# Kernel optimization log

Hardware: AMD Instinct MI355X
Metric: run time of the kernel (lower is better)

## Reference

```python
import jax, jax.numpy as jnp
import numpy as np

DN = ('NCHW', 'OIHW', 'NCHW')
K = 7          # window_size
PAD = K // 2   # 3
GC = 32
CIN = 1
COUT = 3
DIM = 128
RED = DIM // 4  # reduction=4 -> 32


def conv3x3(x, w, b):
    out = jax.lax.conv_general_dilated(x, w, (1, 1), [(1, 1), (1, 1)],
                                       dimension_numbers=DN)
    return out + b[None, :, None, None]


def lrelu(x):
    return jnp.where(x >= 0, x, 0.2 * x)


def setup_inputs() -> dict:
    key = jax.random.key(0)
    ks = jax.random.split(key, 18)
    def n(k, shape, s=0.05):
        return jax.random.normal(k, shape, dtype=jnp.float32) * s
    return {
        'x': jax.random.normal(ks[0], (8, CIN, 256, 256), dtype=jnp.float32),
        'c1_w': n(ks[1], (GC, CIN, 3, 3)),            'c1_b': n(ks[2], (GC,)),
        'c2_w': n(ks[3], (GC, CIN + GC, 3, 3)),       'c2_b': n(ks[4], (GC,)),
        'c3_w': n(ks[5], (GC, CIN + 2 * GC, 3, 3)),   'c3_b': n(ks[6], (GC,)),
        'c4_w': n(ks[7], (GC - 1, CIN + 3 * GC, 3, 3)), 'c4_b': n(ks[8], (GC - 1,)),
        # DynamicDWConv squeeze-excite weight generator
        'dw_w1': n(ks[9], (RED, DIM)),                # 1x1 conv, no bias
        'dw_bn_g': jnp.ones((RED,), jnp.float32),      # BN gamma (eval mode)
        'dw_bn_b': jnp.zeros((RED,), jnp.float32),     # BN beta
        'dw_w2': n(ks[10], (DIM * K * K, RED)),        'dw_b2': n(ks[11], (DIM * K * K,)),
        'dw_bias': n(ks[12], (DIM,)),                  # per-channel bias of depthwise conv
        'c5_w': n(ks[13], (COUT, DIM, 3, 3)),          'c5_b': n(ks[14], (COUT,)),
    }


def reference(x, c1_w, c1_b, c2_w, c2_b, c3_w, c3_b, c4_w, c4_b,
              dw_w1, dw_bn_g, dw_bn_b, dw_w2, dw_b2, dw_bias, c5_w, c5_b):
    # residual dense block
    x1 = lrelu(conv3x3(x, c1_w, c1_b))
    x2 = lrelu(conv3x3(jnp.concatenate((x, x1), 1), c2_w, c2_b))
    x3 = lrelu(conv3x3(jnp.concatenate((x, x1, x2), 1), c3_w, c3_b))
    x4 = lrelu(conv3x3(jnp.concatenate((x, x1, x2, x3), 1), c4_w, c4_b))
    feat = jnp.concatenate((x, x1, x2, x3, x4), 1)  # [b, 128, h, w]
    b = feat.shape[0]

    # DynamicDWConv: generate per-sample depthwise kernels via squeeze-excite
    pooled = feat.mean(axis=(2, 3))                            # [b, 128]
    h = jax.nn.relu(pooled @ dw_w1.T * dw_bn_g + dw_bn_b)      # BN(eval: mean=0,var=1)
    wgen = h @ dw_w2.T + dw_b2                                 # [b, 128*K*K]
    wdw = wgen.reshape(b, DIM, 1, K, K)                        # per-sample dw kernels

    def dw_one(xi, wi):  # xi: [128,h,w], wi: [128,1,K,K]
        return jax.lax.conv_general_dilated(
            xi[None], wi, (1, 1), [(PAD, PAD), (PAD, PAD)],
            dimension_numbers=DN, feature_group_count=DIM)[0]

    dw_out = jax.vmap(dw_one)(feat, wdw) + dw_bias[None, :, None, None]
    x45 = lrelu(dw_out)
    return conv3x3(x45, c5_w, c5_b)
```

## Files before the change

### kernel.cpp

```cpp
#include <hip/hip_runtime.h>
#include <hip/hip_bf16.h>


typedef _Float16 f16;
typedef _Float16 f16x2 __attribute__((ext_vector_type(2)));
typedef _Float16 f16x8 __attribute__((ext_vector_type(8)));
typedef float f32x16 __attribute__((ext_vector_type(16)));

#define IMG 256
#define HW 65536
#define CH 128

static __device__ __forceinline__ size_t fidx(int b, int h, int w) {
    return (((size_t)b * IMG + h) * IMG + w) * CH;
}

__global__ __launch_bounds__(256) void prep_wt_k(const float* __restrict__ src,
                                                 f16* __restrict__ dst,
                                                 int Cin, int COUT) {
    int idx = blockIdx.x * 256 + threadIdx.x;
    if (idx >= 9 * 32 * 128) return;
    int tap = idx >> 12;
    int oc  = (idx >> 7) & 31;
    int pc  = idx & 127;
    int ic  = (pc == 127) ? 0 : pc + 1;
    float v = 0.f;
    if (oc < COUT && ic < Cin) v = src[(oc * Cin + ic) * 9 + tap];
    dst[idx] = (f16)v;
}

__global__ __launch_bounds__(256) void conv1_k(const float* __restrict__ x,
                                               f16* __restrict__ feat,
                                               const float* __restrict__ w,
                                               const float* __restrict__ bias) {
    int wx = threadIdx.x, h = blockIdx.x & 255, b = blockIdx.x >> 8;
    const float* p = x + (size_t)b * HW + h * IMG;
    bool hm = h > 0, hp = h < 255, wm = wx > 0, wp = wx < 255;
    float v[9];
    v[0] = (hm && wm) ? p[wx - 1 - IMG] : 0.f;
    v[1] = hm ? p[wx - IMG] : 0.f;
    v[2] = (hm && wp) ? p[wx + 1 - IMG] : 0.f;
    v[3] = wm ? p[wx - 1] : 0.f;
    v[4] = p[wx];
    v[5] = wp ? p[wx + 1] : 0.f;
    v[6] = (hp && wm) ? p[wx - 1 + IMG] : 0.f;
    v[7] = hp ? p[wx + IMG] : 0.f;
    v[8] = (hp && wp) ? p[wx + 1 + IMG] : 0.f;

    float acc[32];
#pragma unroll
    for (int oc = 0; oc < 32; ++oc) {
        float s = bias[oc];
#pragma unroll
        for (int k = 0; k < 9; ++k) s = fmaf(v[k], w[oc * 9 + k], s);
        acc[oc] = (s >= 0.f) ? s : 0.2f * s;
    }
    f16* op = feat + fidx(b, h, wx);
#pragma unroll
    for (int oc = 0; oc < 32; oc += 2) {
        f16x2 pr = {(f16)acc[oc], (f16)acc[oc + 1]};
        *(f16x2*)(op + oc) = pr;
    }
    op[127] = (f16)v[4];
}

#define NSTT 10
#define STT (18 * 34 * 32)

__device__ __forceinline__ void stage_issue_t(const f16* __restrict__ src,
                                              int b, int r0, int w0, int c0,
                                              int tid, f16x8* v) {
#pragma unroll
    for (int it = 0; it < NSTT; ++it) {
        int u = tid + it * 256;
        int r = u / 136, rem = u - r * 136;
        int slot = rem >> 2, cg = rem & 3;
        int gh = r0 - 1 + r, gw = w0 - 1 + slot;
        bool ok = (u < 2448) && ((unsigned)gh < 256u) && ((unsigned)gw < 256u);
        int ch = gh < 0 ? 0 : (gh > 255 ? 255 : gh);
        int cw = gw < 0 ? 0 : (gw > 255 ? 255 : gw);
        f16x8 t = *(const f16x8*)(src + fidx(b, ch, cw) + c0 + cg * 8);
        f16x8 z = {};
        v[it] = ok ? t : z;
    }
}

__device__ __forceinline__ void stage_write_t(f16* __restrict__ St, int tid,
                                              const f16x8* v) {
#pragma unroll
    for (int it = 0; it < NSTT; ++it) {
        int u = tid + it * 256;
        if (u < 2448) {
            int r = u / 136, rem = u - r * 136;
            int slot = rem >> 2, cg = rem & 3;
            *(f16x8*)(St + ((r * 34 + slot) * 4 + (cg ^ ((slot >> 1) & 3))) * 8) = v[it];
        }
    }
}

__device__ __forceinline__ void compute_t(const f16* __restrict__ St,
                                          const f16* __restrict__ Wt, int c0,
                                          int wave, int l31, int g,
                                          f32x16* acc) {
#pragma unroll
    for (int kx = 0; kx < 3; ++kx) {
        f16x8 A0[3], A1[3];
#pragma unroll
        for (int ky = 0; ky < 3; ++ky) {
            const f16* wp = Wt + ((ky * 3 + kx) * 32 + l31) * 128 + c0 + g * 8;
            A0[ky] = *(const f16x8*)(wp);
            A1[ky] = *(const f16x8*)(wp + 16);
        }
        int slot = l31 + kx;
        int sw = (slot >> 1) & 3;
        int base = wave * 4;
        f16x8 B0[3], B1[3];
#pragma unroll
        for (int i = 0; i < 2; ++i) {
            int rb = ((base + i) * 34 + slot) * 4;
            B0[i] = *(const f16x8*)(St + (rb + ((0 + g) ^ sw)) * 8);
            B1[i] = *(const f16x8*)(St + (rb + ((2 + g) ^ sw)) * 8);
        }
#pragma unroll
        for (int r = 0; r < 4; ++r) {
            int rb = ((base + r + 2) * 34 + slot) * 4;
            B0[(r + 2) % 3] = *(const f16x8*)(St + (rb + ((0 + g) ^ sw)) * 8);
            B1[(r + 2) % 3] = *(const f16x8*)(St + (rb + ((2 + g) ^ sw)) * 8);
#pragma unroll
            for (int ky = 0; ky < 3; ++ky) {
                acc[r] = __builtin_amdgcn_mfma_f32_32x32x16_f16(A0[ky], B0[(r + ky) % 3], acc[r], 0, 0, 0);
                acc[r] = __builtin_amdgcn_mfma_f32_32x32x16_f16(A1[ky], B1[(r + ky) % 3], acc[r], 0, 0, 0);
            }
        }
    }
}

__global__ __launch_bounds__(256, 2) void convm_k(f16* __restrict__ feat,
                                                  const f16* __restrict__ Wt,
                                                  const float* __restrict__ bias,
                                                  int outbase, int cmask, int COUT) {
    __shared__ f16 St[STT];
    int tid = threadIdx.x;
    int wave = tid >> 6, lane = tid & 63;
    int l31 = lane & 31, g = lane >> 5;
    int bi = blockIdx.x;
    int b = bi & 7;
    int tile = bi >> 3;
    int pxt = tile & 7, rt = tile >> 3;
    int r0 = rt * 16;
    int w0 = pxt * 32;
    f32x16 acc[4] = {{}, {}, {}, {}};

    for (int ck = 0; ck < 4; ++ck) {
        if (!((cmask >> ck) & 1)) continue;
        int c0 = ck * 32;
        f16x8 v[NSTT];
        stage_issue_t(feat, b, r0, w0, c0, tid, v);
        stage_write_t(St, tid, v);
        __syncthreads();
        compute_t(St, Wt, c0, wave, l31, g, acc);
        __syncthreads();
    }

    int px = w0 + l31;
#pragma unroll
    for (int r = 0; r < 4; ++r) {
        f16* op = feat + fidx(b, r0 + wave * 4 + r, px) + outbase;
#pragma unroll
        for (int q = 0; q < 16; q += 2) {
            int oc0 = (q & 3) + 8 * (q >> 2) + 4 * g;
            float b0v = bias[oc0];
            float b1v = (oc0 + 1 < COUT) ? bias[oc0 + 1] : 0.f;
            float v0 = acc[r][q] + b0v;
            float v1 = acc[r][q + 1] + b1v;
            v0 = (v0 >= 0.f) ? v0 : 0.2f * v0;
            v1 = (v1 >= 0.f) ? v1 : 0.2f * v1;
            if (oc0 + 1 < COUT) {
                f16x2 pr = {(f16)v0, (f16)v1};
                *(f16x2*)(op + oc0) = pr;
            } else if (oc0 < COUT) {
                op[oc0] = (f16)v0;
            }
        }
    }
}

__global__ __launch_bounds__(256, 2) void convm_out_k(const f16* __restrict__ x45,
                                                      const f16* __restrict__ Wt,
                                                      const float* __restrict__ bias,
                                                      float* __restrict__ out,
                                                      int b0) {
    __shared__ f16 St[STT];
    int tid = threadIdx.x;
    int wave = tid >> 6, lane = tid & 63;
    int l31 = lane & 31, g = lane >> 5;
    int bi = blockIdx.x;
    int bl = bi & 3;
    int tile = bi >> 2;
    int pxt = tile & 7, rt = tile >> 3;
    int r0 = rt * 16;
    int w0 = pxt * 32;
    f32x16 acc[4] = {{}, {}, {}, {}};

    for (int ck = 0; ck < 4; ++ck) {
        int c0 = ck * 32;
        f16x8 v[NSTT];
        stage_issue_t(x45, bl, r0, w0, c0, tid, v);
        stage_write_t(St, tid, v);
        __syncthreads();
        compute_t(St, Wt, c0, wave, l31, g, acc);
        __syncthreads();
    }

    if (g == 0) {
        int gb = b0 + bl;
        int px = w0 + l31;
#pragma unroll
        for (int r = 0; r < 4; ++r) {
#pragma unroll
            for (int oc = 0; oc < 3; ++oc) {
                float vv = acc[r][oc] + bias[oc];
                out[((size_t)(gb * 3 + oc)) * HW
                    + (size_t)(r0 + wave * 4 + r) * IMG + px] = vv;
            }
        }
    }
}

__global__ __launch_bounds__(256, 4) void dw_k(const f16* __restrict__ feat,
                                               const float* __restrict__ wgen,
                                               const float* __restrict__ dwb,
                                               f16* __restrict__ x45,
                                               int b0) {
    int tid = threadIdx.x;
    int lane = tid & 63;
    int wv = tid >> 6;
    int c = (wv & 1) * 64 + lane;
    int colh = wv >> 1;

    int bi = blockIdx.x;
    int ct = bi & 31;
    int t2 = bi >> 5;
    int vt = t2 & 7;
    int bl = t2 >> 3;
    int gb = b0 + bl;
    int x0 = ct * 8 + colh * 4;
    int y0 = vt * 32;

    int lc = (c == 127) ? 0 : c + 1;
    const float* wp = wgen + gb * 6272 + lc;
    f16x2 wp2[7][4];
#pragma unroll
    for (int k = 0; k < 7; ++k) {
#pragma unroll
        for (int p = 0; p < 3; ++p) {
            f16x2 t = {(f16)wp[(k * 7 + 2 * p) * 128],
                       (f16)wp[(k * 7 + 2 * p + 1) * 128]};
            wp2[k][p] = t;
        }
        f16x2 t3 = {(f16)wp[(k * 7 + 6) * 128], (f16)0.f};
        wp2[k][3] = t3;
    }
    float bias = dwb[lc];

    const f16* fb = feat + (size_t)gb * HW * CH + c;
    f16* xb = x45 + (size_t)bl * HW * CH + c;

    int xo[10];
    bool xm[10];
#pragma unroll
    for (int i = 0; i < 10; ++i) {
        int gx = x0 - 3 + i;
        xm[i] = (unsigned)gx < 256u;
        int cx = gx < 0 ? 0 : (gx > 255 ? 255 : gx);
        xo[i] = cx * CH;
    }

    float a[7][4] = {};

    for (int yi = 0; yi < 40; yi += 2) {
        int gy0 = y0 - 3 + yi, gy1 = gy0 + 1;
        bool ym0 = (unsigned)gy0 < 256u, ym1 = (unsigned)gy1 < 256u;
        int cy0 = gy0 < 0 ? 0 : (gy0 > 255 ? 255 : gy0);
        int cy1 = gy1 < 0 ? 0 : (gy1 > 255 ? 255 : gy1);
        const f16* r0 = fb + (size_t)cy0 * IMG * CH;
        const f16* r1 = fb + (size_t)cy1 * IMG * CH;

        f16 u0[10], u1[10];
#pragma unroll
        for (int i = 0; i < 10; ++i) u0[i] = r0[xo[i]];
#pragma unroll
        for (int i = 0; i < 10; ++i) u1[i] = r1[xo[i]];
#pragma unroll
        for (int i = 0; i < 10; ++i) {
            if (!(ym0 && xm[i])) u0[i] = (f16)0.f;
            if (!(ym1 && xm[i])) u1[i] = (f16)0.f;
        }

        {
            f16x2 pe[5], po[5];
#pragma unroll
            for (int p = 0; p < 5; ++p) { f16x2 t = {u0[2 * p], u0[2 * p + 1]}; pe[p] = t; }
#pragma unroll
            for (int p = 0; p < 4; ++p) { f16x2 t = {u0[2 * p + 1], u0[2 * p + 2]}; po[p] = t; }
            { f16x2 t = {u0[9], (f16)0.f}; po[4] = t; }
#pragma unroll
            for (int k = 0; k < 7; ++k) {
                const int wr = 6 - k;
#pragma unroll
                for (int p = 0; p < 4; ++p) {
                    a[k][0] = __builtin_amdgcn_fdot2(pe[p],     wp2[wr][p], a[k][0], false);
                    a[k][1] = __builtin_amdgcn_fdot2(po[p],     wp2[wr][p], a[k][1], false);
                    a[k][2] = __builtin_amdgcn_fdot2(pe[p + 1], wp2[wr][p], a[k][2], false);
                    a[k][3] = __builtin_amdgcn_fdot2(po[p + 1], wp2[wr][p], a[k][3], false);
                }
            }
            if (yi >= 6 && yi < 38) {
                int yo = y0 + yi - 6;
#pragma unroll
                for (int j = 0; j < 4; ++j) {
                    float s = a[0][j] + bias;
                    s = (s >= 0.f) ? s : 0.2f * s;
                    xb[((size_t)yo * IMG + x0 + j) * CH] = (f16)s;
                }
            }
#pragma unroll
            for (int k = 0; k < 6; ++k)
#pragma unroll
                for (int j = 0; j < 4; ++j) a[k][j] = a[k + 1][j];
#pragma unroll
            for (int j = 0; j < 4; ++j) a[6][j] = 0.f;
        }

        {
            f16x2 pe[5], po[5];
#pragma unroll
            for (int p = 0; p < 5; ++p) { f16x2 t = {u1[2 * p], u1[2 * p + 1]}; pe[p] = t; }
#pragma unroll
            for (int p = 0; p < 4; ++p) { f16x2 t = {u1[2 * p + 1], u1[2 * p + 2]}; po[p] = t; }
            { f16x2 t = {u1[9], (f16)0.f}; po[4] = t; }
#pragma unroll
            for (int k = 0; k < 7; ++k) {
                const int wr = 6 - k;
#pragma unroll
                for (int p = 0; p < 4; ++p) {
                    a[k][0] = __builtin_amdgcn_fdot2(pe[p],     wp2[wr][p], a[k][0], false);
                    a[k][1] = __builtin_amdgcn_fdot2(po[p],     wp2[wr][p], a[k][1], false);
                    a[k][2] = __builtin_amdgcn_fdot2(pe[p + 1], wp2[wr][p], a[k][2], false);
                    a[k][3] = __builtin_amdgcn_fdot2(po[p + 1], wp2[wr][p], a[k][3], false);
                }
            }
            int yib = yi + 1;
            if (yib >= 6 && yib < 38) {
                int yo = y0 + yib - 6;
#pragma unroll
                for (int j = 0; j < 4; ++j) {
                    float s = a[0][j] + bias;
                    s = (s >= 0.f) ? s : 0.2f * s;
                    xb[((size_t)yo * IMG + x0 + j) * CH] = (f16)s;
                }
            }
#pragma unroll
            for (int k = 0; k < 6; ++k)
#pragma unroll
                for (int j = 0; j < 4; ++j) a[k][j] = a[k + 1][j];
#pragma unroll
            for (int j = 0; j < 4; ++j) a[6][j] = 0.f;
        }
    }
}

__global__ __launch_bounds__(256) void pool_part_k(const f16* __restrict__ feat,
                                                   float* __restrict__ part) {
    __shared__ float red[4][128];
    int bi = blockIdx.x;
    int b = bi >> 5, pb = bi & 31;
    int t = threadIdx.x;
    int cp = t & 63, ps = t >> 6;
    int px0 = pb * 2048 + ps * 512;
    float s0 = 0.f, s1 = 0.f;
    const f16* base = feat + (size_t)b * HW * CH + (size_t)px0 * CH + cp * 2;
    for (int i = 0; i < 512; ++i) {
        f16x2 v = *(const f16x2*)(base + (size_t)i * CH);
        s0 += (float)v[0];
        s1 += (float)v[1];
    }
    red[ps][cp * 2] = s0;
    red[ps][cp * 2 + 1] = s1;
    __syncthreads();
    if (t < 128) {
        float s = red[0][t] + red[1][t] + red[2][t] + red[3][t];
        part[((size_t)b * 32 + pb) * 128 + t] = s;
    }
}

__global__ __launch_bounds__(256) void pool_fin_k(const float* __restrict__ part,
                                                  float* __restrict__ pooled) {
    int gid = blockIdx.x * 256 + threadIdx.x;
    if (gid >= 1024) return;
    int b = gid >> 7, pc = gid & 127;
    float s = 0.f;
    for (int pb = 0; pb < 32; ++pb) s += part[((size_t)b * 32 + pb) * 128 + pc];
    int lc = (pc == 127) ? 0 : pc + 1;
    pooled[b * 128 + lc] = s * (1.f / 65536.f);
}

__global__ __launch_bounds__(256) void mlp1_k(const float* __restrict__ pooled,
                                              const float* __restrict__ w1,
                                              const float* __restrict__ g,
                                              const float* __restrict__ bb,
                                              float* __restrict__ hbuf) {
    int t = threadIdx.x;
    int b = t >> 5, r = t & 31;
    float s = 0.f;
    for (int c = 0; c < 128; ++c) s += pooled[b * 128 + c] * w1[r * 128 + c];
    s = s * g[r] + bb[r];
    hbuf[t] = (s > 0.f) ? s : 0.f;
}

__global__ __launch_bounds__(256) void mlp2_k(const float* __restrict__ hbuf,
                                              const float* __restrict__ w2,
                                              const float* __restrict__ b2,
                                              float* __restrict__ wgen) {
    int idx = blockIdx.x * 256 + threadIdx.x;
    if (idx >= 8 * 6272) return;
    int b = idx / 6272, i = idx - b * 6272;
    float s = b2[i];
    for (int r = 0; r < 32; ++r) s += hbuf[b * 32 + r] * w2[i * 32 + r];
    int lc = i / 49, tp = i - lc * 49;
    wgen[b * 6272 + tp * 128 + lc] = s;
}

extern "C" void kernel_launch(void* const* d_in, const int* in_sizes, int n_in,
                              void* d_out, int out_size, void* d_ws, size_t ws_size,
                              hipStream_t stream) {
    (void)in_sizes; (void)n_in; (void)out_size; (void)ws_size;
    const float* x     = (const float*)d_in[0];
    const float* c1w   = (const float*)d_in[1];
    const float* c1b   = (const float*)d_in[2];
    const float* c2w   = (const float*)d_in[3];
    const float* c2b   = (const float*)d_in[4];
    const float* c3w   = (const float*)d_in[5];
    const float* c3b   = (const float*)d_in[6];
    const float* c4w   = (const float*)d_in[7];
    const float* c4b   = (const float*)d_in[8];
    const float* dw_w1 = (const float*)d_in[9];
    const float* bn_g  = (const float*)d_in[10];
    const float* bn_b  = (const float*)d_in[11];
    const float* dw_w2 = (const float*)d_in[12];
    const float* dw_b2 = (const float*)d_in[13];
    const float* dwb   = (const float*)d_in[14];
    const float* c5w   = (const float*)d_in[15];
    const float* c5b   = (const float*)d_in[16];
    float* out = (float*)d_out;

    f16* feat = (f16*)d_ws;
    f16* x45  = feat + (size_t)8 * HW * CH;
    f16* Wt   = x45 + (size_t)4 * HW * CH;
    f16* Wt2 = Wt, *Wt3 = Wt + 36864, *Wt4 = Wt + 73728, *Wt5 = Wt + 110592;
    float* part   = (float*)(Wt + 4 * 36864);
    float* pooled = part + 8 * 32 * 128;
    float* hbuf   = pooled + 1024;
    float* wgen   = hbuf + 256;

    prep_wt_k<<<144, 256, 0, stream>>>(c2w, Wt2, 33, 32);
    prep_wt_k<<<144, 256, 0, stream>>>(c3w, Wt3, 65, 32);
    prep_wt_k<<<144, 256, 0, stream>>>(c4w, Wt4, 97, 31);
    prep_wt_k<<<144, 256, 0, stream>>>(c5w, Wt5, 128, 3);

    conv1_k<<<2048, 256, 0, stream>>>(x, feat, c1w, c1b);
    convm_k<<<1024, 256, 0, stream>>>(feat, Wt2, c2b, 32, 0b1001, 32);
    convm_k<<<1024, 256, 0, stream>>>(feat, Wt3, c3b, 64, 0b1011, 32);
    convm_k<<<1024, 256, 0, stream>>>(feat, Wt4, c4b, 96, 0b1111, 31);

    pool_part_k<<<256, 256, 0, stream>>>(feat, part);
    pool_fin_k<<<4, 256, 0, stream>>>(part, pooled);
    mlp1_k<<<1, 256, 0, stream>>>(pooled, dw_w1, bn_g, bn_b, hbuf);
    mlp2_k<<<196, 256, 0, stream>>>(hbuf, dw_w2, dw_b2, wgen);

    for (int b0 = 0; b0 < 8; b0 += 4) {
        dw_k<<<1024, 256, 0, stream>>>(feat, wgen, dwb, x45, b0);
        convm_out_k<<<512, 256, 0, stream>>>(x45, Wt5, c5b, out, b0);
    }
}
```

Measured before the change: 468.8 us.

## Drop LDS staging in MFMA 3x3 convs and load B operands directly from global

The 3x3 conv kernels no longer stage an 18x34 halo tile of each 32-channel slice into shared memory with block barriers. Each wave now loads its B operands straight from global memory (served by L1/L2), using a rolling 6-row window per kx tap and boundary masking. Occupancy hint goes from 2 to 3 blocks per SM, since no LDS is used. The aim is to remove barrier stalls and LDS traffic, at the cost of redundant global/cache loads across waves and taps and less latency hiding.

```diff
diff --git a/kernel.cpp b/kernel.cpp
--- a/kernel.cpp
+++ b/kernel.cpp
@@ -64,82 +64,56 @@
     op[127] = (f16)v[4];
 }
 
-#define NSTT 10
-#define STT (18 * 34 * 32)
-
-__device__ __forceinline__ void stage_issue_t(const f16* __restrict__ src,
-                                              int b, int r0, int w0, int c0,
-                                              int tid, f16x8* v) {
-#pragma unroll
-    for (int it = 0; it < NSTT; ++it) {
-        int u = tid + it * 256;
-        int r = u / 136, rem = u - r * 136;
-        int slot = rem >> 2, cg = rem & 3;
-        int gh = r0 - 1 + r, gw = w0 - 1 + slot;
-        bool ok = (u < 2448) && ((unsigned)gh < 256u) && ((unsigned)gw < 256u);
-        int ch = gh < 0 ? 0 : (gh > 255 ? 255 : gh);
-        int cw = gw < 0 ? 0 : (gw > 255 ? 255 : gw);
-        f16x8 t = *(const f16x8*)(src + fidx(b, ch, cw) + c0 + cg * 8);
-        f16x8 z = {};
-        v[it] = ok ? t : z;
-    }
-}
-
-__device__ __forceinline__ void stage_write_t(f16* __restrict__ St, int tid,
-                                              const f16x8* v) {
-#pragma unroll
-    for (int it = 0; it < NSTT; ++it) {
-        int u = tid + it * 256;
-        if (u < 2448) {
-            int r = u / 136, rem = u - r * 136;
-            int slot = rem >> 2, cg = rem & 3;
-            *(f16x8*)(St + ((r * 34 + slot) * 4 + (cg ^ ((slot >> 1) & 3))) * 8) = v[it];
-        }
-    }
-}
-
-__device__ __forceinline__ void compute_t(const f16* __restrict__ St,
-                                          const f16* __restrict__ Wt, int c0,
-                                          int wave, int l31, int g,
+
+__device__ __forceinline__ void conv_core(const f16* __restrict__ src,
+                                          const f16* __restrict__ Wt,
+                                          int b, int R, int w0,
+                                          int cmask, int l31, int g,
                                           f32x16* acc) {
-#pragma unroll
-    for (int kx = 0; kx < 3; ++kx) {
-        f16x8 A0[3], A1[3];
-#pragma unroll
-        for (int ky = 0; ky < 3; ++ky) {
-            const f16* wp = Wt + ((ky * 3 + kx) * 32 + l31) * 128 + c0 + g * 8;
-            A0[ky] = *(const f16x8*)(wp);
-            A1[ky] = *(const f16x8*)(wp + 16);
-        }
-        int slot = l31 + kx;
-        int sw = (slot >> 1) & 3;
-        int base = wave * 4;
-        f16x8 B0[3], B1[3];
-#pragma unroll
-        for (int i = 0; i < 2; ++i) {
-            int rb = ((base + i) * 34 + slot) * 4;
-            B0[i] = *(const f16x8*)(St + (rb + ((0 + g) ^ sw)) * 8);
-            B1[i] = *(const f16x8*)(St + (rb + ((2 + g) ^ sw)) * 8);
-        }
-#pragma unroll
-        for (int r = 0; r < 4; ++r) {
-            int rb = ((base + r + 2) * 34 + slot) * 4;
-            B0[(r + 2) % 3] = *(const f16x8*)(St + (rb + ((0 + g) ^ sw)) * 8);
-            B1[(r + 2) % 3] = *(const f16x8*)(St + (rb + ((2 + g) ^ sw)) * 8);
+    for (int ck = 0; ck < 4; ++ck) {
+        if (!((cmask >> ck) & 1)) continue;
+        int c0 = ck * 32;
+#pragma unroll
+        for (int kx = 0; kx < 3; ++kx) {
+            f16x8 A0[3], A1[3];
 #pragma unroll
             for (int ky = 0; ky < 3; ++ky) {
-                acc[r] = __builtin_amdgcn_mfma_f32_32x32x16_f16(A0[ky], B0[(r + ky) % 3], acc[r], 0, 0, 0);
-                acc[r] = __builtin_amdgcn_mfma_f32_32x32x16_f16(A1[ky], B1[(r + ky) % 3], acc[r], 0, 0, 0);
-            }
-        }
-    }
-}
-
-__global__ __launch_bounds__(256, 2) void convm_k(f16* __restrict__ feat,
+                const f16* wp = Wt + ((ky * 3 + kx) * 32 + l31) * 128 + c0 + g * 8;
+                A0[ky] = *(const f16x8*)(wp);
+                A1[ky] = *(const f16x8*)(wp + 16);
+            }
+            int px = w0 + l31 + kx - 1;
+            bool xok = (unsigned)px < 256u;
+            int cpx = px < 0 ? 0 : (px > 255 ? 255 : px);
+#pragma unroll
+            for (int ri = 0; ri < 6; ++ri) {
+                int row = R - 1 + ri;
+                bool yok = (unsigned)row < 256u;
+                int crow = row < 0 ? 0 : (row > 255 ? 255 : row);
+                const f16* p = src + fidx(b, crow, cpx) + c0 + g * 8;
+                f16x8 B0 = *(const f16x8*)(p);
+                f16x8 B1 = *(const f16x8*)(p + 16);
+                f16x8 z = {};
+                bool ok = xok && yok;
+                B0 = ok ? B0 : z;
+                B1 = ok ? B1 : z;
+#pragma unroll
+                for (int ky = 0; ky < 3; ++ky) {
+                    int r = ri - ky;
+                    if (r >= 0 && r < 4) {
+                        acc[r] = __builtin_amdgcn_mfma_f32_32x32x16_f16(A0[ky], B0, acc[r], 0, 0, 0);
+                        acc[r] = __builtin_amdgcn_mfma_f32_32x32x16_f16(A1[ky], B1, acc[r], 0, 0, 0);
+                    }
+                }
+            }
+        }
+    }
+}
+
+__global__ __launch_bounds__(256, 3) void convm_k(f16* __restrict__ feat,
                                                   const f16* __restrict__ Wt,
                                                   const float* __restrict__ bias,
                                                   int outbase, int cmask, int COUT) {
-    __shared__ f16 St[STT];
     int tid = threadIdx.x;
     int wave = tid >> 6, lane = tid & 63;
     int l31 = lane & 31, g = lane >> 5;
@@ -149,23 +123,15 @@
     int pxt = tile & 7, rt = tile >> 3;
     int r0 = rt * 16;
     int w0 = pxt * 32;
+    int R = r0 + wave * 4;
     f32x16 acc[4] = {{}, {}, {}, {}};
 
-    for (int ck = 0; ck < 4; ++ck) {
-        if (!((cmask >> ck) & 1)) continue;
-        int c0 = ck * 32;
-        f16x8 v[NSTT];
-        stage_issue_t(feat, b, r0, w0, c0, tid, v);
-        stage_write_t(St, tid, v);
-        __syncthreads();
-        compute_t(St, Wt, c0, wave, l31, g, acc);
-        __syncthreads();
-    }
+    conv_core(feat, Wt, b, R, w0, cmask, l31, g, acc);
 
     int px = w0 + l31;
 #pragma unroll
     for (int r = 0; r < 4; ++r) {
-        f16* op = feat + fidx(b, r0 + wave * 4 + r, px) + outbase;
+        f16* op = feat + fidx(b, R + r, px) + outbase;
 #pragma unroll
         for (int q = 0; q < 16; q += 2) {
             int oc0 = (q & 3) + 8 * (q >> 2) + 4 * g;
@@ -185,12 +151,11 @@
     }
 }
 
-__global__ __launch_bounds__(256, 2) void convm_out_k(const f16* __restrict__ x45,
+__global__ __launch_bounds__(256, 3) void convm_out_k(const f16* __restrict__ x45,
                                                       const f16* __restrict__ Wt,
                                                       const float* __restrict__ bias,
                                                       float* __restrict__ out,
                                                       int b0) {
-    __shared__ f16 St[STT];
     int tid = threadIdx.x;
     int wave = tid >> 6, lane = tid & 63;
     int l31 = lane & 31, g = lane >> 5;
@@ -200,17 +165,10 @@
     int pxt = tile & 7, rt = tile >> 3;
     int r0 = rt * 16;
     int w0 = pxt * 32;
+    int R = r0 + wave * 4;
     f32x16 acc[4] = {{}, {}, {}, {}};
 
-    for (int ck = 0; ck < 4; ++ck) {
-        int c0 = ck * 32;
-        f16x8 v[NSTT];
-        stage_issue_t(x45, bl, r0, w0, c0, tid, v);
-        stage_write_t(St, tid, v);
-        __syncthreads();
-        compute_t(St, Wt, c0, wave, l31, g, acc);
-        __syncthreads();
-    }
+    conv_core(x45, Wt, bl, R, w0, 0b1111, l31, g, acc);
 
     if (g == 0) {
         int gb = b0 + bl;
@@ -220,8 +178,7 @@
 #pragma unroll
             for (int oc = 0; oc < 3; ++oc) {
                 float vv = acc[r][oc] + bias[oc];
-                out[((size_t)(gb * 3 + oc)) * HW
-                    + (size_t)(r0 + wave * 4 + r) * IMG + px] = vv;
+                out[((size_t)(gb * 3 + oc)) * HW + (size_t)(R + r) * IMG + px] = vv;
             }
         }
     }
```

After: 784.8 us. 1.67x slower.

## Stage conv tiles via direct global-to-LDS loads and raise occupancy

Applied to the files above, without the earlier changes.

Replaces register-staged global loads plus LDS writes with __builtin_amdgcn_global_load_lds, which copies 16-byte chunks straight into shared memory. The swizzle moves from the LDS address to the source address so each lane writes linearly. Out-of-bounds halo cells are zeroed once per block for edge tiles, and launch bounds rise to 4 blocks per CU since the staging registers are gone. This removes the VGPR round trip and frees registers, but relies on halo zeros surviving across channel chunks and on the compiler placing a correct wait before the barrier.

```diff
diff --git a/kernel.cpp b/kernel.cpp
--- a/kernel.cpp
+++ b/kernel.cpp
@@ -1,5 +1,6 @@
 #include <hip/hip_runtime.h>
 #include <hip/hip_bf16.h>
+#include <stdint.h>
 
 
 typedef _Float16 f16;
@@ -67,33 +68,46 @@
 #define NSTT 10
 #define STT (18 * 34 * 32)
 
-__device__ __forceinline__ void stage_issue_t(const f16* __restrict__ src,
-                                              int b, int r0, int w0, int c0,
-                                              int tid, f16x8* v) {
+typedef const uint32_t __attribute__((address_space(1)))* gas1_t;
+typedef uint32_t __attribute__((address_space(3)))* las3_t;
+
+__device__ __forceinline__ void zero_oob_t(f16* __restrict__ St,
+                                           int r0, int w0, int tid) {
+    bool edge = (r0 == 0) || (r0 == 240) || (w0 == 0) || (w0 == 224);
+    if (edge) {
+        f16x8 z = {};
+#pragma unroll
+        for (int it = 0; it < NSTT; ++it) {
+            int u = tid + it * 256;
+            if (u < 2448) {
+                int r = u / 136, rem = u - r * 136;
+                int slot = rem >> 2;
+                int gh = r0 - 1 + r, gw = w0 - 1 + slot;
+                if (!((unsigned)gh < 256u && (unsigned)gw < 256u))
+                    *(f16x8*)(St + (size_t)u * 8) = z;
+            }
+        }
+    }
+}
+
+__device__ __forceinline__ void stage_gll_t(const f16* __restrict__ src,
+                                            f16* __restrict__ St,
+                                            int b, int r0, int w0, int c0,
+                                            int wave, int lane) {
 #pragma unroll
     for (int it = 0; it < NSTT; ++it) {
-        int u = tid + it * 256;
-        int r = u / 136, rem = u - r * 136;
-        int slot = rem >> 2, cg = rem & 3;
-        int gh = r0 - 1 + r, gw = w0 - 1 + slot;
-        bool ok = (u < 2448) && ((unsigned)gh < 256u) && ((unsigned)gw < 256u);
-        int ch = gh < 0 ? 0 : (gh > 255 ? 255 : gh);
-        int cw = gw < 0 ? 0 : (gw > 255 ? 255 : gw);
-        f16x8 t = *(const f16x8*)(src + fidx(b, ch, cw) + c0 + cg * 8);
-        f16x8 z = {};
-        v[it] = ok ? t : z;
-    }
-}
-
-__device__ __forceinline__ void stage_write_t(f16* __restrict__ St, int tid,
-                                              const f16x8* v) {
-#pragma unroll
-    for (int it = 0; it < NSTT; ++it) {
-        int u = tid + it * 256;
+        int ubase = it * 256 + wave * 64;
+        int u = ubase + lane;
+        f16* lp = St + (size_t)ubase * 8;
         if (u < 2448) {
             int r = u / 136, rem = u - r * 136;
-            int slot = rem >> 2, cg = rem & 3;
-            *(f16x8*)(St + ((r * 34 + slot) * 4 + (cg ^ ((slot >> 1) & 3))) * 8) = v[it];
+            int slot = rem >> 2, cgl = rem & 3;
+            int cg = cgl ^ ((slot >> 1) & 3);
+            int gh = r0 - 1 + r, gw = w0 - 1 + slot;
+            if ((unsigned)gh < 256u && (unsigned)gw < 256u) {
+                const f16* gp = src + fidx(b, gh, gw) + c0 + cg * 8;
+                __builtin_amdgcn_global_load_lds((gas1_t)gp, (las3_t)lp, 16, 0, 0);
+            }
         }
     }
 }
@@ -135,7 +149,7 @@
     }
 }
 
-__global__ __launch_bounds__(256, 2) void convm_k(f16* __restrict__ feat,
+__global__ __launch_bounds__(256, 4) void convm_k(f16* __restrict__ feat,
                                                   const f16* __restrict__ Wt,
                                                   const float* __restrict__ bias,
                                                   int outbase, int cmask, int COUT) {
@@ -151,12 +165,13 @@
     int w0 = pxt * 32;
     f32x16 acc[4] = {{}, {}, {}, {}};
 
+    zero_oob_t(St, r0, w0, tid);
+    __syncthreads();
+
     for (int ck = 0; ck < 4; ++ck) {
         if (!((cmask >> ck) & 1)) continue;
         int c0 = ck * 32;
-        f16x8 v[NSTT];
-        stage_issue_t(feat, b, r0, w0, c0, tid, v);
-        stage_write_t(St, tid, v);
+        stage_gll_t(feat, St, b, r0, w0, c0, wave, lane);
         __syncthreads();
         compute_t(St, Wt, c0, wave, l31, g, acc);
         __syncthreads();
@@ -185,7 +200,7 @@
     }
 }
 
-__global__ __launch_bounds__(256, 2) void convm_out_k(const f16* __restrict__ x45,
+__global__ __launch_bounds__(256, 4) void convm_out_k(const f16* __restrict__ x45,
                                                       const f16* __restrict__ Wt,
                                                       const float* __restrict__ bias,
                                                       float* __restrict__ out,
@@ -202,11 +217,12 @@
     int w0 = pxt * 32;
     f32x16 acc[4] = {{}, {}, {}, {}};
 
+    zero_oob_t(St, r0, w0, tid);
+    __syncthreads();
+
     for (int ck = 0; ck < 4; ++ck) {
         int c0 = ck * 32;
-        f16x8 v[NSTT];
-        stage_issue_t(x45, bl, r0, w0, c0, tid, v);
-        stage_write_t(St, tid, v);
+        stage_gll_t(x45, St, bl, r0, w0, c0, wave, lane);
         __syncthreads();
         compute_t(St, Wt, c0, wave, l31, g, acc);
         __syncthreads();
```

Result: slower. 653.3 us (+39.4%).

## Double-buffer LDS staging in conv kernels to overlap loads with MFMA compute

Applied to the files above, without the earlier changes.

Both 3x3 MFMA conv kernels now use two shared-memory tile buffers. The global loads for the next 32-channel chunk are issued before computing the current chunk and written to the other buffer afterward, leaving one barrier per iteration. This is meant to hide global-memory latency behind MFMA work. The cost is double the LDS footprint and extra registers held across the compute, which may reduce occupancy under launch_bounds(256,2).

```diff
diff --git a/kernel.cpp b/kernel.cpp
--- a/kernel.cpp
+++ b/kernel.cpp
@@ -139,7 +139,7 @@
                                                   const f16* __restrict__ Wt,
                                                   const float* __restrict__ bias,
                                                   int outbase, int cmask, int COUT) {
-    __shared__ f16 St[STT];
+    __shared__ f16 St[2][STT];
     int tid = threadIdx.x;
     int wave = tid >> 6, lane = tid & 63;
     int l31 = lane & 31, g = lane >> 5;
@@ -151,14 +151,25 @@
     int w0 = pxt * 32;
     f32x16 acc[4] = {{}, {}, {}, {}};
 
-    for (int ck = 0; ck < 4; ++ck) {
-        if (!((cmask >> ck) & 1)) continue;
-        int c0 = ck * 32;
+    int cks[4], ncs = 0;
+#pragma unroll
+    for (int i = 0; i < 4; ++i)
+        if ((cmask >> i) & 1) cks[ncs++] = i;
+
+    {
         f16x8 v[NSTT];
-        stage_issue_t(feat, b, r0, w0, c0, tid, v);
-        stage_write_t(St, tid, v);
-        __syncthreads();
-        compute_t(St, Wt, c0, wave, l31, g, acc);
+        stage_issue_t(feat, b, r0, w0, cks[0] * 32, tid, v);
+        stage_write_t(St[0], tid, v);
+    }
+    __syncthreads();
+
+    for (int i = 0; i < ncs; ++i) {
+        f16x8 vn[NSTT];
+        if (i + 1 < ncs)
+            stage_issue_t(feat, b, r0, w0, cks[i + 1] * 32, tid, vn);
+        compute_t(St[i & 1], Wt, cks[i] * 32, wave, l31, g, acc);
+        if (i + 1 < ncs)
+            stage_write_t(St[(i + 1) & 1], tid, vn);
         __syncthreads();
     }
 
@@ -190,7 +201,7 @@
                                                       const float* __restrict__ bias,
                                                       float* __restrict__ out,
                                                       int b0) {
-    __shared__ f16 St[STT];
+    __shared__ f16 St[2][STT];
     int tid = threadIdx.x;
     int wave = tid >> 6, lane = tid & 63;
     int l31 = lane & 31, g = lane >> 5;
@@ -202,13 +213,20 @@
     int w0 = pxt * 32;
     f32x16 acc[4] = {{}, {}, {}, {}};
 
-    for (int ck = 0; ck < 4; ++ck) {
-        int c0 = ck * 32;
+    {
         f16x8 v[NSTT];
-        stage_issue_t(x45, bl, r0, w0, c0, tid, v);
-        stage_write_t(St, tid, v);
-        __syncthreads();
-        compute_t(St, Wt, c0, wave, l31, g, acc);
+        stage_issue_t(x45, bl, r0, w0, 0, tid, v);
+        stage_write_t(St[0], tid, v);
+    }
+    __syncthreads();
+
+    for (int i = 0; i < 4; ++i) {
+        f16x8 vn[NSTT];
+        if (i + 1 < 4)
+            stage_issue_t(x45, bl, r0, w0, (i + 1) * 32, tid, vn);
+        compute_t(St[i & 1], Wt, i * 32, wave, l31, g, acc);
+        if (i + 1 < 4)
+            stage_write_t(St[(i + 1) & 1], tid, vn);
         __syncthreads();
     }
 
```

After: 463.9 us. About the same (-1.0%).
